# Performance work log

Hardware: AMD Instinct MI355X
Metric: run time of the kernel (lower is better)

Reference implementation:

```python
import jax, jax.numpy as jnp
import numpy as np

N_NODES = 20000
T_STEPS = 8


def _layer_norm(x, g, b, eps=1e-5):
    mu = x.mean(-1, keepdims=True)
    var = ((x - mu) ** 2).mean(-1, keepdims=True)
    return (x - mu) * jax.lax.rsqrt(var + eps) * g + b


def _linear(x, W, b):
    # torch nn.Linear: x @ W.T + b, W is [out, in]
    return x @ W.T + b


def _gcn_conv(xw, norm, src, dst, b, n):
    # xw: pre-transformed features [N, H]; symmetric-normalized aggregation
    msg = xw[src] * norm[:, None]
    return jax.ops.segment_sum(msg, dst, num_segments=n) + b


def setup_inputs() -> dict:
    key = jax.random.key(0)
    ks = jax.random.split(key, 16)
    N, T, K, E, D, H, M = N_NODES, T_STEPS, 4000, 400000, 128, 128, 16
    s = 0.05
    return {
        "node_t": jax.random.randint(ks[0], (T, K), 0, N),
        "edge_index_t": jax.random.randint(ks[1], (T, 2, E), 0, N),
        "m": M,
        "emb": jax.random.normal(ks[2], (N, D), jnp.float32) * s,
        "convW1": jax.random.normal(ks[3], (H, D), jnp.float32) * s,
        "convb1": jnp.zeros((H,), jnp.float32),
        "convW2": jax.random.normal(ks[4], (H, H), jnp.float32) * s,
        "convb2": jnp.zeros((H,), jnp.float32),
        "tn_g": jnp.ones((H,), jnp.float32),
        "tn_b": jnp.zeros((H,), jnp.float32),
        "tok_w1": jax.random.normal(ks[5], (M, M), jnp.float32) * s,
        "tok_b1": jnp.zeros((M,), jnp.float32),
        "tok_w2": jax.random.normal(ks[6], (M, M), jnp.float32) * s,
        "tok_b2": jnp.zeros((M,), jnp.float32),
        "cn_g": jnp.ones((H,), jnp.float32),
        "cn_b": jnp.zeros((H,), jnp.float32),
        "ch_w1": jax.random.normal(ks[7], (H, H), jnp.float32) * s,
        "ch_b1": jnp.zeros((H,), jnp.float32),
        "ch_w2": jax.random.normal(ks[8], (H, H), jnp.float32) * s,
        "ch_b2": jnp.zeros((H,), jnp.float32),
    }


def reference(node_t, edge_index_t, m, emb, convW1, convb1, convW2, convb2,
              tn_g, tn_b, tok_w1, tok_b1, tok_w2, tok_b2,
              cn_g, cn_b, ch_w1, ch_b1, ch_w2, ch_b2):
    N = emb.shape[0]
    H = convW1.shape[0]
    gelu = lambda x: jax.nn.gelu(x, approximate=False)

    def mixer(x):  # x: [N, m, H]
        y = _layer_norm(x, tn_g, tn_b)
        y = jnp.swapaxes(y, 1, 2)                 # [N, H, m]
        y = _linear(gelu(_linear(y, tok_w1, tok_b1)), tok_w2, tok_b2)
        x = x + jnp.swapaxes(y, 1, 2)
        z = _layer_norm(x, cn_g, cn_b)
        z = _linear(gelu(_linear(z, ch_w1, ch_b1)), ch_w2, ch_b2)
        return x + z

    # conv linear transforms are per-node dense and constant w.r.t. step input emb
    xw1 = emb @ convW1.T                          # [N, H]
    self_loop = jnp.arange(N)

    def step(x_m, xs):
        node_i, edge_i = xs                        # [K], [2, E]
        x_m_new = mixer(x_m)
        x_new = x_m_new.mean(axis=1)               # FinalProcessLayer, discrete
        # GCN with self-loops and symmetric normalization
        src = jnp.concatenate([edge_i[0], self_loop])
        dst = jnp.concatenate([edge_i[1], self_loop])
        deg = jax.ops.segment_sum(jnp.ones_like(src, jnp.float32), dst,
                                  num_segments=N)
        dinv = jax.lax.rsqrt(jnp.maximum(deg, 1.0))
        norm = dinv[src] * dinv[dst]
        h = _gcn_conv(xw1, norm, src, dst, convb1, N)
        h = jax.nn.relu(h)
        h = _gcn_conv(h @ convW2.T, norm, src, dst, convb2, N)
        # zero rows of nodes present at this timestep (boolean-mask scatter)
        h = h.at[node_i].set(0.0)
        # slide window
        x_m = jnp.concatenate([x_m[:, 1:, :], h[:, None, :]], axis=1)
        return x_m, x_new

    x_m0 = jnp.zeros((N, m, H), jnp.float32)
    _, outs = jax.lax.scan(step, x_m0, (node_t, edge_index_t))
    return outs  # [T, N, H]
```

## Files before the change

### kernel.cpp

```cpp
#include <hip/hip_runtime.h>
#include <hip/hip_bf16.h>
#include <cstdint>
#include <cstddef>

#define NN 20000
#define HH 128
#define MM 16
#define KK 4000
#define EE 400000

typedef __attribute__((ext_vector_type(16))) float f16v;
typedef __attribute__((ext_vector_type(8))) short short8;
typedef __attribute__((ext_vector_type(4))) float f32x4;
typedef __attribute__((ext_vector_type(8), may_alias)) short s8ma;
typedef __attribute__((ext_vector_type(4), may_alias)) float f4ma;

__device__ __forceinline__ float gelu_f(float x) {
  return 0.5f * x * (1.0f + erff(x * 0.70710678118654752440f));
}

__device__ __forceinline__ unsigned short f2bf(float f) {
  union { float f; unsigned u; } v; v.f = f;
  unsigned u = v.u;
  unsigned r = (u + 0x7FFFu + ((u >> 16) & 1u)) >> 16;
  return (unsigned short)r;
}
__device__ __forceinline__ float bf2f(unsigned short s) {
  union { unsigned u; float f; } v; v.u = ((unsigned)s) << 16; return v.f;
}


__global__ void zero1_kernel(int* __restrict__ a, int n) {
  int i = blockIdx.x * 256 + threadIdx.x;
  if (i < n) a[i] = 0;
}

__global__ void count7_kernel(const int* __restrict__ edges, int* __restrict__ cnt7, int n7) {
  int e = blockIdx.x * 256 + threadIdx.x;
  if (e < n7) {
    int t = e / EE, i = e - t * EE;
    int d = edges[(size_t)t * 2 * EE + EE + i];
    atomicAdd(&cnt7[t * NN + d], 1);
  }
}

__global__ void dinv_kernel(const int* __restrict__ cnt, float* __restrict__ dinv, int n) {
  int i = blockIdx.x * 256 + threadIdx.x;
  if (i < n) dinv[i] = rsqrtf((float)(cnt[i] + 1));
}

__global__ void scan7_kernel(const int* __restrict__ cnt7, int* __restrict__ offs7) {
  __shared__ int sh[1024];
  __shared__ int carry_s;
  const int b = blockIdx.x;
  const int* cnt = cnt7 + b * NN;
  int* offs = offs7 + b * (NN + 1);
  int tid = threadIdx.x;
  if (tid == 0) carry_s = 0;
  __syncthreads();
  for (int base = 0; base < NN; base += 1024) {
    int i = base + tid;
    int v = (i < NN) ? cnt[i] : 0;
    sh[tid] = v;
    __syncthreads();
    for (int off = 1; off < 1024; off <<= 1) {
      int t = (tid >= off) ? sh[tid - off] : 0;
      __syncthreads();
      sh[tid] += t;
      __syncthreads();
    }
    int carry = carry_s;
    if (i < NN) offs[i] = carry + sh[tid] - v;
    __syncthreads();
    if (tid == 1023) carry_s = carry + sh[1023];
    __syncthreads();
  }
  if (tid == 0) offs[NN] = carry_s;
}

__global__ void fillcsr7_kernel(const int* __restrict__ edges,
                                const int* __restrict__ offs7, int* __restrict__ cursor7,
                                const float* __restrict__ dinv7,
                                int* __restrict__ csrc7, float* __restrict__ cnorm7, int n7) {
  int e = blockIdx.x * 256 + threadIdx.x;
  if (e < n7) {
    int t = e / EE, i = e - t * EE;
    const int* es = edges + (size_t)t * 2 * EE;
    int s = es[i], d = es[EE + i];
    int pos = offs7[t * (NN + 1) + d] + atomicAdd(&cursor7[t * NN + d], 1);
    csrc7[(size_t)t * EE + pos] = s;
    cnorm7[(size_t)t * EE + pos] = dinv7[t * NN + s] * dinv7[t * NN + d];
  }
}

__global__ __launch_bounds__(128) void agg7_kernel(const float* __restrict__ X,
    const int* __restrict__ csrc7, const float* __restrict__ cnorm7,
    const int* __restrict__ offs7, const float* __restrict__ dinv7,
    const float* __restrict__ bias, int relu, float* __restrict__ Y, int xshared) {
  const int b = blockIdx.x;
  const int t = b / NN, i = b - t * NN;
  const int c = threadIdx.x;
  const int* csrc = csrc7 + (size_t)t * EE;
  const float* cnorm = cnorm7 + (size_t)t * EE;
  const int* offs = offs7 + t * (NN + 1);
  const float* dinv = dinv7 + t * NN;
  const float* Xt = xshared ? X : X + (size_t)t * NN * HH;
  float di = dinv[i];
  float acc = Xt[(size_t)i * HH + c] * di * di;
  int s0 = offs[i], e0 = offs[i + 1];
  for (int j = s0; j < e0; ++j) {
    acc += Xt[(size_t)csrc[j] * HH + c] * cnorm[j];
  }
  acc += bias[c];
  if (relu) acc = fmaxf(acc, 0.f);
  Y[(size_t)b * HH + c] = acc;
}

__global__ __launch_bounds__(128) void gemm128_kernel(const float* __restrict__ X,
    const float* __restrict__ W, float* __restrict__ Y, int nrows) {
  __shared__ float Ws[128 * 129];
  __shared__ float Xs[8 * 128];
  int tid = threadIdx.x;
  for (int idx = tid; idx < 16384; idx += 128) {
    int o = idx >> 7, k = idx & 127;
    Ws[o * 129 + k] = W[idx];
  }
  __syncthreads();
  for (int row0 = blockIdx.x * 8; row0 < nrows; row0 += gridDim.x * 8) {
    int nr = min(8, nrows - row0);
    for (int idx = tid; idx < nr * 128; idx += 128) Xs[idx] = X[(size_t)row0 * 128 + idx];
    __syncthreads();
    float acc[8] = {0, 0, 0, 0, 0, 0, 0, 0};
    for (int k = 0; k < 128; ++k) {
      float w = Ws[tid * 129 + k];
#pragma unroll
      for (int r = 0; r < 8; ++r) acc[r] += w * Xs[r * 128 + k];
    }
    for (int r = 0; r < nr; ++r) Y[(size_t)(row0 + r) * 128 + tid] = acc[r];
    __syncthreads();
  }
}

__global__ void mask7_kernel(const int* __restrict__ node_t, float* __restrict__ hb, int n) {
  int idx = blockIdx.x * 256 + threadIdx.x;
  if (idx < n) {
    int t = idx / (KK * HH), r = idx - t * KK * HH;
    int j = r >> 7, c = r & 127;
    hb[((size_t)t * NN + node_t[t * KK + j]) * HH + c] = 0.f;
  }
}

__global__ void bcast_kernel(float* __restrict__ out, int total) {
  int idx = blockIdx.x * 256 + threadIdx.x + 128;
  if (idx < total) out[idx] = out[idx & 127];
}

__global__ void wprep_kernel(const float* __restrict__ w1, const float* __restrict__ w2,
                             unsigned short* __restrict__ b1, unsigned short* __restrict__ b2) {
  int i = blockIdx.x * 256 + threadIdx.x;
  if (i < 16384) { b1[i] = f2bf(w1[i]); b2[i] = f2bf(w2[i]); }
}


__global__ __launch_bounds__(256, 2) void mixA_kernel(
    const float* __restrict__ hbufs,
    const float* __restrict__ tn_g, const float* __restrict__ tn_b,
    const float* __restrict__ tok_w1, const float* __restrict__ tok_b1,
    const float* __restrict__ tok_w2, const float* __restrict__ tok_b2,
    const float* __restrict__ cn_g, const float* __restrict__ cn_b,
    unsigned short* __restrict__ zh_g, unsigned short* __restrict__ zl_g,
    float* __restrict__ fout_g, int total_items, int item4s, int niter) {
  __shared__ __align__(16) float zw[64 * 132];
  __shared__ float tg[128], tbv[128], cg[128], cbv[128];
  __shared__ float tw1s[256], tw2s[256], tb1s[16], tb2s[16];

  const int tid = threadIdx.x;
  if (tid < 128) {
    tg[tid] = tn_g[tid]; tbv[tid] = tn_b[tid];
    cg[tid] = cn_g[tid]; cbv[tid] = cn_b[tid];
  }
  tw1s[tid] = tok_w1[tid];
  tw2s[tid] = tok_w2[tid];
  if (tid < 16) { tb1s[tid] = tok_b1[tid]; tb2s[tid] = tok_b2[tid]; }
  __syncthreads();

  const int lr = tid >> 2;
  const int lq = tid & 3;
  const int c2 = tid & 127;
  const int n0 = tid >> 7;

  for (int it = 0; it < niter; ++it) {
    const int item4 = it * gridDim.x + blockIdx.x;
    if (item4 >= item4s) break;

    {
      const int n = lr >> 4, tok = lr & 15;
      const int item = item4 * 4 + n;
      const bool act = item < total_items;
      int t = 0, node = 0;
      if (act && item < 7 * NN) { t = item / NN + 1; node = item % NN; }
      int src_t = tok - (MM - t);
      f4ma x[8];
      if (act && src_t >= 0) {
        const float* hp = hbufs + ((size_t)src_t * NN + node) * HH + lq * 32;
#pragma unroll
        for (int j = 0; j < 8; ++j) x[j] = *(const f4ma*)(hp + 4 * j);
      } else {
#pragma unroll
        for (int j = 0; j < 8; ++j) x[j] = (f4ma){0.f, 0.f, 0.f, 0.f};
      }
      float s = 0.f, ss = 0.f;
#pragma unroll
      for (int j = 0; j < 8; ++j) {
        s += x[j].x + x[j].y + x[j].z + x[j].w;
        ss += x[j].x * x[j].x + x[j].y * x[j].y + x[j].z * x[j].z + x[j].w * x[j].w;
      }
      s += __shfl_xor(s, 1); ss += __shfl_xor(ss, 1);
      s += __shfl_xor(s, 2); ss += __shfl_xor(ss, 2);
      float mu = s * (1.f / 128.f);
      float var = fmaxf(ss * (1.f / 128.f) - mu * mu, 0.f);
      float rs = rsqrtf(var + 1e-5f);
#pragma unroll
      for (int j = 0; j < 8; ++j) *(f4ma*)&zw[lr * 132 + lq * 32 + 4 * j] = x[j];
      if (lq == 0) { zw[lr * 132 + 128] = mu; zw[lr * 132 + 129] = rs; }
    }
    __syncthreads();

    {
      const int rb0 = n0 * 16 * 132, rb1 = (n0 + 2) * 16 * 132;
      const float tgc = tg[c2], tbc = tbv[c2];
      f16v a0v, a1v;
#pragma unroll
      for (int hd = 0; hd < 16; ++hd) { float b = tb1s[hd]; a0v[hd] = b; a1v[hd] = b; }
#pragma unroll
      for (int r = 0; r < 16; ++r) {
        float x0 = zw[rb0 + r * 132 + c2];
        float m0 = zw[rb0 + r * 132 + 128], q0 = zw[rb0 + r * 132 + 129];
        float x1 = zw[rb1 + r * 132 + c2];
        float m1 = zw[rb1 + r * 132 + 128], q1 = zw[rb1 + r * 132 + 129];
        float z0 = (x0 - m0) * q0 * tgc + tbc;
        float z1 = (x1 - m1) * q1 * tgc + tbc;
#pragma unroll
        for (int hd = 0; hd < 16; ++hd) {
          float w = tw1s[hd * 16 + r];
          a0v[hd] += w * z0; a1v[hd] += w * z1;
        }
      }
#pragma unroll
      for (int hd = 0; hd < 16; ++hd) { a0v[hd] = gelu_f(a0v[hd]); a1v[hd] = gelu_f(a1v[hd]); }
      float cs0 = 0.f, cs1 = 0.f;
#pragma unroll
      for (int r = 0; r < 16; ++r) {
        float o0 = tb2s[r], o1 = tb2s[r];
#pragma unroll
        for (int hd = 0; hd < 16; ++hd) {
          float w = tw2s[r * 16 + hd];
          o0 += w * a0v[hd]; o1 += w * a1v[hd];
        }
        float nx0 = zw[rb0 + r * 132 + c2] + o0;
        float nx1 = zw[rb1 + r * 132 + c2] + o1;
        cs0 += nx0; cs1 += nx1;
        zw[rb0 + r * 132 + c2] = nx0;
        zw[rb1 + r * 132 + c2] = nx1;
      }
      fout_g[(size_t)(item4 * 4 + n0) * 128 + c2] = cs0;
      fout_g[(size_t)(item4 * 4 + n0 + 2) * 128 + c2] = cs1;
    }
    __syncthreads();

    {
      f4ma x[8];
#pragma unroll
      for (int j = 0; j < 8; ++j) x[j] = *(const f4ma*)&zw[lr * 132 + lq * 32 + 4 * j];
      float s = 0.f, ss = 0.f;
#pragma unroll
      for (int j = 0; j < 8; ++j) {
        s += x[j].x + x[j].y + x[j].z + x[j].w;
        ss += x[j].x * x[j].x + x[j].y * x[j].y + x[j].z * x[j].z + x[j].w * x[j].w;
      }
      s += __shfl_xor(s, 1); ss += __shfl_xor(ss, 1);
      s += __shfl_xor(s, 2); ss += __shfl_xor(ss, 2);
      float mu = s * (1.f / 128.f);
      float var = fmaxf(ss * (1.f / 128.f) - mu * mu, 0.f);
      float rs = rsqrtf(var + 1e-5f);
      const size_t g0 = (size_t)item4 * 64 * 128 + (size_t)lr * 128;
#pragma unroll
      for (int j = 0; j < 4; ++j) {
        int c0 = lq * 32 + 8 * j;
        short8 ph, pl;
#pragma unroll
        for (int e = 0; e < 8; ++e) {
          int c = c0 + e;
          float xe = (e < 4) ? ((const float*)&x[2 * j])[e] : ((const float*)&x[2 * j + 1])[e - 4];
          float zf = (xe - mu) * rs * cg[c] + cbv[c];
          unsigned short hi = f2bf(zf);
          ph[e] = (short)hi;
          pl[e] = (short)f2bf(zf - bf2f(hi));
        }
        *(s8ma*)&zh_g[g0 + c0] = (s8ma)ph;
        *(s8ma*)&zl_g[g0 + c0] = (s8ma)pl;
      }
    }
    __syncthreads();
  }
}


__global__ __launch_bounds__(256, 2) void mixB_kernel(
    const unsigned short* __restrict__ zh_g, const unsigned short* __restrict__ zl_g,
    const float* __restrict__ fout_g,
    const unsigned short* __restrict__ wbf1, const unsigned short* __restrict__ wbf2,
    const float* __restrict__ ch_b1, const float* __restrict__ ch_b2,
    float* __restrict__ out, int total_items, int item4s, int niter) {
  __shared__ __align__(16) unsigned short zh[64 * 136];
  __shared__ __align__(16) unsigned short zl[64 * 136];
  __shared__ float cb1v[128], cb2v[128];

  const int tid = threadIdx.x;
  const int lane = tid & 63;
  const int wv = tid >> 6;
  const int q = lane >> 4;
  const int h = lane & 15;
  if (tid < 128) { cb1v[tid] = ch_b1[tid]; cb2v[tid] = ch_b2[tid]; }
  __syncthreads();

  const int wbase0 = ((2 * wv) * 16 + h) * 128 + q * 8;
  const int wbase1 = ((2 * wv + 1) * 16 + h) * 128 + q * 8;
  const int srow = tid >> 2;
  const int scq = tid & 3;

  for (int it = 0; it < niter; ++it) {
    const int item4 = it * gridDim.x + blockIdx.x;
    if (item4 >= item4s) break;

    {
      const size_t g0 = (size_t)item4 * 64 * 128 + (size_t)srow * 128 + scq * 32;
#pragma unroll
      for (int j = 0; j < 4; ++j) {
        *(s8ma*)&zh[srow * 136 + scq * 32 + 8 * j] = *(const s8ma*)&zh_g[g0 + 8 * j];
        *(s8ma*)&zl[srow * 136 + scq * 32 + 8 * j] = *(const s8ma*)&zl_g[g0 + 8 * j];
      }
    }
    __syncthreads();

    asm volatile("" ::: "memory");
    {
      short8 wf[4][2];
#pragma unroll
      for (int ks = 0; ks < 4; ++ks) {
        wf[ks][0] = (short8)(*(const s8ma*)&wbf1[wbase0 + ks * 32]);
        wf[ks][1] = (short8)(*(const s8ma*)&wbf1[wbase1 + ks * 32]);
      }
      f32x4 acc[4][2];
#pragma unroll
      for (int rt = 0; rt < 4; ++rt) {
#pragma unroll
        for (int j = 0; j < 2; ++j) {
          float b = cb1v[(2 * wv + j) * 16 + h];
          acc[rt][j] = (f32x4){b, b, b, b};
        }
      }
#pragma unroll
      for (int ks = 0; ks < 4; ++ks) {
        const int col = ks * 32 + q * 8;
#pragma unroll
        for (int rt = 0; rt < 4; ++rt) {
          short8 ah = (short8)(*(const s8ma*)&zh[(rt * 16 + h) * 136 + col]);
          short8 al = (short8)(*(const s8ma*)&zl[(rt * 16 + h) * 136 + col]);
#pragma unroll
          for (int j = 0; j < 2; ++j) {
            acc[rt][j] = __builtin_amdgcn_mfma_f32_16x16x32_bf16(ah, wf[ks][j], acc[rt][j], 0, 0, 0);
            acc[rt][j] = __builtin_amdgcn_mfma_f32_16x16x32_bf16(al, wf[ks][j], acc[rt][j], 0, 0, 0);
          }
        }
      }
      __syncthreads();
#pragma unroll
      for (int rt = 0; rt < 4; ++rt) {
#pragma unroll
        for (int j = 0; j < 2; ++j) {
          int col = (2 * wv + j) * 16 + h;
#pragma unroll
          for (int rg = 0; rg < 4; ++rg) {
            int row = rt * 16 + q * 4 + rg;
            float v = gelu_f(acc[rt][j][rg]);
            unsigned short hi = f2bf(v);
            zh[row * 136 + col] = hi;
            zl[row * 136 + col] = f2bf(v - bf2f(hi));
          }
        }
      }
    }
    __syncthreads();

    asm volatile("" ::: "memory");
    {
      short8 wf[4][2];
#pragma unroll
      for (int ks = 0; ks < 4; ++ks) {
        wf[ks][0] = (short8)(*(const s8ma*)&wbf2[wbase0 + ks * 32]);
        wf[ks][1] = (short8)(*(const s8ma*)&wbf2[wbase1 + ks * 32]);
      }
      f32x4 acc[4][2];
#pragma unroll
      for (int rt = 0; rt < 4; ++rt) {
#pragma unroll
        for (int j = 0; j < 2; ++j) {
          float b = cb2v[(2 * wv + j) * 16 + h];
          acc[rt][j] = (f32x4){b, b, b, b};
        }
      }
#pragma unroll
      for (int ks = 0; ks < 4; ++ks) {
        const int col = ks * 32 + q * 8;
#pragma unroll
        for (int rt = 0; rt < 4; ++rt) {
          short8 ah = (short8)(*(const s8ma*)&zh[(rt * 16 + h) * 136 + col]);
          short8 al = (short8)(*(const s8ma*)&zl[(rt * 16 + h) * 136 + col]);
#pragma unroll
          for (int j = 0; j < 2; ++j) {
            acc[rt][j] = __builtin_amdgcn_mfma_f32_16x16x32_bf16(ah, wf[ks][j], acc[rt][j], 0, 0, 0);
            acc[rt][j] = __builtin_amdgcn_mfma_f32_16x16x32_bf16(al, wf[ks][j], acc[rt][j], 0, 0, 0);
          }
        }
      }
#pragma unroll
      for (int rt = 0; rt < 4; ++rt) {
        const int item = item4 * 4 + rt;
        const bool act = item < total_items;
        int t = 0, node = 0;
        if (act && item < 7 * NN) { t = item / NN + 1; node = item % NN; }
#pragma unroll
        for (int j = 0; j < 2; ++j) {
          float v = acc[rt][j][0] + acc[rt][j][1] + acc[rt][j][2] + acc[rt][j][3];
          v += __shfl_xor(v, 16);
          v += __shfl_xor(v, 32);
          if (q == 0 && act) {
            int col = (2 * wv + j) * 16 + h;
            out[((size_t)t * NN + node) * HH + col] =
                (fout_g[(size_t)item * 128 + col] + v) * (1.f / 16.f);
          }
        }
      }
    }
    __syncthreads();
  }
}


__global__ __launch_bounds__(256) void mixer16_kernel(
    const float* __restrict__ hbufs,
    const float* __restrict__ tn_g, const float* __restrict__ tn_b,
    const float* __restrict__ tok_w1, const float* __restrict__ tok_b1,
    const float* __restrict__ tok_w2, const float* __restrict__ tok_b2,
    const float* __restrict__ cn_g, const float* __restrict__ cn_b,
    const float* __restrict__ ch_w1, const float* __restrict__ ch_b1,
    const float* __restrict__ ch_w2, const float* __restrict__ ch_b2,
    float* __restrict__ out, int total_items, int niter) {
  __shared__ __align__(16) float zw[64 * 132];
  __shared__ __align__(16) unsigned short zh[64 * 136];
  __shared__ __align__(16) unsigned short zl[64 * 136];
  __shared__ float fout[4 * 128];
  __shared__ float tg[128], tbv[128], cg[128], cbv[128], cb1v[128], cb2v[128];
  __shared__ float tw1s[256], tw2s[256], tb1s[16], tb2s[16];

  const int tid = threadIdx.x;
  const int lane = tid & 63;
  const int wv = tid >> 6;
  const int q = lane >> 4;
  const int h = lane & 15;

  if (tid < 128) {
    tg[tid] = tn_g[tid]; tbv[tid] = tn_b[tid];
    cg[tid] = cn_g[tid]; cbv[tid] = cn_b[tid];
    cb1v[tid] = ch_b1[tid]; cb2v[tid] = ch_b2[tid];
  }
  tw1s[tid] = tok_w1[tid];
  tw2s[tid] = tok_w2[tid];
  if (tid < 16) { tb1s[tid] = tok_b1[tid]; tb2s[tid] = tok_b2[tid]; }

  short8 wf1[4][2], wf2[4][2];
#pragma unroll
  for (int ks = 0; ks < 4; ++ks) {
#pragma unroll
    for (int j = 0; j < 2; ++j) {
      int o = (2 * wv + j) * 16 + h;
      int k0 = ks * 32 + q * 8;
      const float* s1 = ch_w1 + o * 128 + k0;
      const float* s2 = ch_w2 + o * 128 + k0;
      short8 p1, p2;
#pragma unroll
      for (int e = 0; e < 8; ++e) { p1[e] = (short)f2bf(s1[e]); p2[e] = (short)f2bf(s2[e]); }
      wf1[ks][j] = p1;
      wf2[ks][j] = p2;
    }
  }
  __syncthreads();

  const int lr = tid >> 2;
  const int lq = tid & 3;
  const int c2 = tid & 127;
  const int n0 = tid >> 7;

  for (int it = 0; it < niter; ++it) {
    const int item4 = it * gridDim.x + blockIdx.x;

    {
      const int n = lr >> 4, tok = lr & 15;
      const int item = item4 * 4 + n;
      const bool act = item < total_items;
      int t = 0, node = 0;
      if (act && item < 7 * NN) { t = item / NN + 1; node = item % NN; }
      int src_t = tok - (MM - t);
      f4ma x[8];
      if (act && src_t >= 0) {
        const float* hp = hbufs + ((size_t)src_t * NN + node) * HH + lq * 32;
#pragma unroll
        for (int j = 0; j < 8; ++j) x[j] = *(const f4ma*)(hp + 4 * j);
      } else {
#pragma unroll
        for (int j = 0; j < 8; ++j) x[j] = (f4ma){0.f, 0.f, 0.f, 0.f};
      }
      float s = 0.f, ss = 0.f;
#pragma unroll
      for (int j = 0; j < 8; ++j) {
        s += x[j].x + x[j].y + x[j].z + x[j].w;
        ss += x[j].x * x[j].x + x[j].y * x[j].y + x[j].z * x[j].z + x[j].w * x[j].w;
      }
      s += __shfl_xor(s, 1); ss += __shfl_xor(ss, 1);
      s += __shfl_xor(s, 2); ss += __shfl_xor(ss, 2);
      float mu = s * (1.f / 128.f);
      float var = fmaxf(ss * (1.f / 128.f) - mu * mu, 0.f);
      float rs = rsqrtf(var + 1e-5f);
#pragma unroll
      for (int j = 0; j < 8; ++j) *(f4ma*)&zw[lr * 132 + lq * 32 + 4 * j] = x[j];
      if (lq == 0) { zw[lr * 132 + 128] = mu; zw[lr * 132 + 129] = rs; }
    }
    __syncthreads();

    {
      const int rb0 = n0 * 16 * 132, rb1 = (n0 + 2) * 16 * 132;
      const float tgc = tg[c2], tbc = tbv[c2];
      f16v a0v, a1v;
#pragma unroll
      for (int hd = 0; hd < 16; ++hd) { float b = tb1s[hd]; a0v[hd] = b; a1v[hd] = b; }
#pragma unroll
      for (int r = 0; r < 16; ++r) {
        float x0 = zw[rb0 + r * 132 + c2];
        float m0 = zw[rb0 + r * 132 + 128], q0 = zw[rb0 + r * 132 + 129];
        float x1 = zw[rb1 + r * 132 + c2];
        float m1 = zw[rb1 + r * 132 + 128], q1 = zw[rb1 + r * 132 + 129];
        float z0 = (x0 - m0) * q0 * tgc + tbc;
        float z1 = (x1 - m1) * q1 * tgc + tbc;
#pragma unroll
        for (int hd = 0; hd < 16; ++hd) {
          float w = tw1s[hd * 16 + r];
          a0v[hd] += w * z0; a1v[hd] += w * z1;
        }
      }
#pragma unroll
      for (int hd = 0; hd < 16; ++hd) { a0v[hd] = gelu_f(a0v[hd]); a1v[hd] = gelu_f(a1v[hd]); }
      float cs0 = 0.f, cs1 = 0.f;
#pragma unroll
      for (int r = 0; r < 16; ++r) {
        float o0 = tb2s[r], o1 = tb2s[r];
#pragma unroll
        for (int hd = 0; hd < 16; ++hd) {
          float w = tw2s[r * 16 + hd];
          o0 += w * a0v[hd]; o1 += w * a1v[hd];
        }
        float nx0 = zw[rb0 + r * 132 + c2] + o0;
        float nx1 = zw[rb1 + r * 132 + c2] + o1;
        cs0 += nx0; cs1 += nx1;
        zw[rb0 + r * 132 + c2] = nx0;
        zw[rb1 + r * 132 + c2] = nx1;
      }
      fout[n0 * 128 + c2] = cs0;
      fout[(n0 + 2) * 128 + c2] = cs1;
    }
    __syncthreads();

    {
      f4ma x[8];
#pragma unroll
      for (int j = 0; j < 8; ++j) x[j] = *(const f4ma*)&zw[lr * 132 + lq * 32 + 4 * j];
      float s = 0.f, ss = 0.f;
#pragma unroll
      for (int j = 0; j < 8; ++j) {
        s += x[j].x + x[j].y + x[j].z + x[j].w;
        ss += x[j].x * x[j].x + x[j].y * x[j].y + x[j].z * x[j].z + x[j].w * x[j].w;
      }
      s += __shfl_xor(s, 1); ss += __shfl_xor(ss, 1);
      s += __shfl_xor(s, 2); ss += __shfl_xor(ss, 2);
      float mu = s * (1.f / 128.f);
      float var = fmaxf(ss * (1.f / 128.f) - mu * mu, 0.f);
      float rs = rsqrtf(var + 1e-5f);
#pragma unroll
      for (int j = 0; j < 4; ++j) {
        int c0 = lq * 32 + 8 * j;
        short8 ph, pl;
#pragma unroll
        for (int e = 0; e < 8; ++e) {
          int c = c0 + e;
          float xe = (e < 4) ? ((const float*)&x[2 * j])[e] : ((const float*)&x[2 * j + 1])[e - 4];
          float zf = (xe - mu) * rs * cg[c] + cbv[c];
          unsigned short hi = f2bf(zf);
          ph[e] = (short)hi;
          pl[e] = (short)f2bf(zf - bf2f(hi));
        }
        *(s8ma*)&zh[lr * 136 + c0] = (s8ma)ph;
        *(s8ma*)&zl[lr * 136 + c0] = (s8ma)pl;
      }
    }
    __syncthreads();

    {
      f32x4 acc[4][2];
#pragma unroll
      for (int rt = 0; rt < 4; ++rt) {
#pragma unroll
        for (int j = 0; j < 2; ++j) {
          float b = cb1v[(2 * wv + j) * 16 + h];
          acc[rt][j] = (f32x4){b, b, b, b};
        }
      }
#pragma unroll
      for (int ks = 0; ks < 4; ++ks) {
        const int col = ks * 32 + q * 8;
#pragma unroll
        for (int rt = 0; rt < 4; ++rt) {
          short8 ah = (short8)(*(const s8ma*)&zh[(rt * 16 + h) * 136 + col]);
          short8 al = (short8)(*(const s8ma*)&zl[(rt * 16 + h) * 136 + col]);
#pragma unroll
          for (int j = 0; j < 2; ++j) {
            acc[rt][j] = __builtin_amdgcn_mfma_f32_16x16x32_bf16(ah, wf1[ks][j], acc[rt][j], 0, 0, 0);
            acc[rt][j] = __builtin_amdgcn_mfma_f32_16x16x32_bf16(al, wf1[ks][j], acc[rt][j], 0, 0, 0);
          }
        }
      }
      __syncthreads();
#pragma unroll
      for (int rt = 0; rt < 4; ++rt) {
#pragma unroll
        for (int j = 0; j < 2; ++j) {
          int col = (2 * wv + j) * 16 + h;
#pragma unroll
          for (int rg = 0; rg < 4; ++rg) {
            int row = rt * 16 + q * 4 + rg;
            float v = gelu_f(acc[rt][j][rg]);
            unsigned short hi = f2bf(v);
            zh[row * 136 + col] = hi;
            zl[row * 136 + col] = f2bf(v - bf2f(hi));
          }
        }
      }
    }
    __syncthreads();

    {
      f32x4 acc[4][2];
#pragma unroll
      for (int rt = 0; rt < 4; ++rt) {
#pragma unroll
        for (int j = 0; j < 2; ++j) {
          float b = cb2v[(2 * wv + j) * 16 + h];
          acc[rt][j] = (f32x4){b, b, b, b};
        }
      }
#pragma unroll
      for (int ks = 0; ks < 4; ++ks) {
        const int col = ks * 32 + q * 8;
#pragma unroll
        for (int rt = 0; rt < 4; ++rt) {
          short8 ah = (short8)(*(const s8ma*)&zh[(rt * 16 + h) * 136 + col]);
          short8 al = (short8)(*(const s8ma*)&zl[(rt * 16 + h) * 136 + col]);
#pragma unroll
          for (int j = 0; j < 2; ++j) {
            acc[rt][j] = __builtin_amdgcn_mfma_f32_16x16x32_bf16(ah, wf2[ks][j], acc[rt][j], 0, 0, 0);
            acc[rt][j] = __builtin_amdgcn_mfma_f32_16x16x32_bf16(al, wf2[ks][j], acc[rt][j], 0, 0, 0);
          }
        }
      }
#pragma unroll
      for (int rt = 0; rt < 4; ++rt) {
        const int item = item4 * 4 + rt;
        const bool act = item < total_items;
        int t = 0, node = 0;
        if (act && item < 7 * NN) { t = item / NN + 1; node = item % NN; }
#pragma unroll
        for (int j = 0; j < 2; ++j) {
          float v = acc[rt][j][0] + acc[rt][j][1] + acc[rt][j][2] + acc[rt][j][3];
          v += __shfl_xor(v, 16);
          v += __shfl_xor(v, 32);
          if (q == 0 && act) {
            int col = (2 * wv + j) * 16 + h;
            out[((size_t)t * NN + node) * HH + col] = (fout[rt * 128 + col] + v) * (1.f / 16.f);
          }
        }
      }
    }
    __syncthreads();
  }
}


extern "C" void kernel_launch(void* const* d_in, const int* in_sizes, int n_in,
                              void* d_out, int out_size, void* d_ws, size_t ws_size,
                              hipStream_t stream) {
  const int* node_t   = (const int*)d_in[0];
  const int* edges    = (const int*)d_in[1];
  const float* emb    = (const float*)d_in[3];
  const float* convW1 = (const float*)d_in[4];
  const float* convb1 = (const float*)d_in[5];
  const float* convW2 = (const float*)d_in[6];
  const float* convb2 = (const float*)d_in[7];
  const float* tn_g   = (const float*)d_in[8];
  const float* tn_b   = (const float*)d_in[9];
  const float* tok_w1 = (const float*)d_in[10];
  const float* tok_b1 = (const float*)d_in[11];
  const float* tok_w2 = (const float*)d_in[12];
  const float* tok_b2 = (const float*)d_in[13];
  const float* cn_g   = (const float*)d_in[14];
  const float* cn_b   = (const float*)d_in[15];
  const float* ch_w1  = (const float*)d_in[16];
  const float* ch_b1  = (const float*)d_in[17];
  const float* ch_w2  = (const float*)d_in[18];
  const float* ch_b2  = (const float*)d_in[19];
  float* out = (float*)d_out;

  char* ws = (char*)d_ws;
  size_t off = 0;
  auto alloc = [&](size_t bytes) -> void* {
    void* p = ws + off;
    off += (bytes + 511) & ~(size_t)511;
    return p;
  };
  float* xw1   = (float*)alloc((size_t)NN * HH * 4);
  float* hbufs = (float*)alloc((size_t)7 * NN * HH * 4);
  int*   cnt7  = (int*)alloc((size_t)7 * NN * 4);
  float* dinv7 = (float*)alloc((size_t)7 * NN * 4);
  int*   offs7 = (int*)alloc((size_t)7 * (NN + 1) * 4);
  int*   cursor7 = (int*)alloc((size_t)7 * NN * 4);
  unsigned short* wbf1 = (unsigned short*)alloc((size_t)16384 * 2);
  unsigned short* wbf2 = (unsigned short*)alloc((size_t)16384 * 2);

  const bool batched = ws_size >= (size_t)260 * 1024 * 1024;
  const bool split   = ws_size >= (size_t)1700 * 1024 * 1024;

  const int total_items = 7 * NN + 1;
  const int item4s = (total_items + 3) / 4;

  gemm128_kernel<<<512, 128, 0, stream>>>(emb, convW1, xw1, NN);
  wprep_kernel<<<64, 256, 0, stream>>>(ch_w1, ch_w2, wbf1, wbf2);

  zero1_kernel<<<(7 * NN + 255) / 256, 256, 0, stream>>>(cnt7, 7 * NN);
  count7_kernel<<<(7 * EE + 255) / 256, 256, 0, stream>>>(edges, cnt7, 7 * EE);
  dinv_kernel<<<(7 * NN + 255) / 256, 256, 0, stream>>>(cnt7, dinv7, 7 * NN);
  scan7_kernel<<<7, 1024, 0, stream>>>(cnt7, offs7);

  if (batched) {
    int*   csrc7  = (int*)alloc((size_t)7 * EE * 4);
    float* cnorm7 = (float*)alloc((size_t)7 * EE * 4);
    float* h7     = (float*)alloc((size_t)7 * NN * HH * 4);
    float* g7     = (float*)alloc((size_t)7 * NN * HH * 4);

    zero1_kernel<<<(7 * NN + 255) / 256, 256, 0, stream>>>(cursor7, 7 * NN);
    fillcsr7_kernel<<<(7 * EE + 255) / 256, 256, 0, stream>>>(edges, offs7, cursor7,
                                                              dinv7, csrc7, cnorm7, 7 * EE);
    agg7_kernel<<<7 * NN, 128, 0, stream>>>(xw1, csrc7, cnorm7, offs7, dinv7,
                                            convb1, 1, h7, 1);
    gemm128_kernel<<<2048, 128, 0, stream>>>(h7, convW2, g7, 7 * NN);
    agg7_kernel<<<7 * NN, 128, 0, stream>>>(g7, csrc7, cnorm7, offs7, dinv7,
                                            convb2, 0, hbufs, 0);
    mask7_kernel<<<(7 * KK * HH + 255) / 256, 256, 0, stream>>>(node_t, hbufs, 7 * KK * HH);
  } else {
    int*   csrc  = (int*)alloc((size_t)EE * 4);
    float* cnorm = (float*)alloc((size_t)EE * 4);
    float* h1    = (float*)alloc((size_t)NN * HH * 4);
    float* g1    = (float*)alloc((size_t)NN * HH * 4);
    for (int t = 0; t < 7; ++t) {
      const int* offs = offs7 + (size_t)t * (NN + 1);
      const float* dinv = dinv7 + (size_t)t * NN;
      zero1_kernel<<<(NN + 255) / 256, 256, 0, stream>>>(cursor7, NN);
      fillcsr7_kernel<<<(EE + 255) / 256, 256, 0, stream>>>(edges + (size_t)t * 2 * EE,
                                                            offs, cursor7, dinv, csrc, cnorm, EE);
      agg7_kernel<<<NN, 128, 0, stream>>>(xw1, csrc, cnorm, offs, dinv, convb1, 1, h1, 1);
      gemm128_kernel<<<512, 128, 0, stream>>>(h1, convW2, g1, NN);
      agg7_kernel<<<NN, 128, 0, stream>>>(g1, csrc, cnorm, offs, dinv, convb2, 0,
                                          hbufs + (size_t)t * NN * HH, 0);
      mask7_kernel<<<(KK * HH + 255) / 256, 256, 0, stream>>>(node_t + (size_t)t * KK,
                                                              hbufs + (size_t)t * NN * HH,
                                                              KK * HH);
    }
  }

  if (split) {
    float* fout_g = (float*)alloc((size_t)item4s * 4 * 128 * 4);
    unsigned short* zh_g = (unsigned short*)alloc((size_t)item4s * 64 * 128 * 2);
    unsigned short* zl_g = (unsigned short*)alloc((size_t)item4s * 64 * 128 * 2);
    const int nblocks = 2048;
    const int niter = (item4s + nblocks - 1) / nblocks;
    mixA_kernel<<<nblocks, 256, 0, stream>>>(hbufs, tn_g, tn_b, tok_w1, tok_b1,
                                             tok_w2, tok_b2, cn_g, cn_b,
                                             zh_g, zl_g, fout_g,
                                             total_items, item4s, niter);
    mixB_kernel<<<nblocks, 256, 0, stream>>>(zh_g, zl_g, fout_g, wbf1, wbf2,
                                             ch_b1, ch_b2, out,
                                             total_items, item4s, niter);
  } else {
    const int nblocks = 2048;
    const int niter = (item4s + nblocks - 1) / nblocks;
    mixer16_kernel<<<nblocks, 256, 0, stream>>>(hbufs, tn_g, tn_b, tok_w1, tok_b1,
                                                tok_w2, tok_b2, cn_g, cn_b, ch_w1, ch_b1,
                                                ch_w2, ch_b2, out, total_items, niter);
  }
  bcast_kernel<<<((NN * HH - 128) + 255) / 256, 256, 0, stream>>>(out, NN * HH);
}
```

Baseline: 3.234 ms.

## Chunk split mixer kernels over reused scratch buffers to enable split path

The split mixA/mixB path used to need a large workspace and otherwise fell back to the fused mixer16 kernel. It now runs in chunks of 4096 item groups per launch pair, storing intermediates in the h7, g7 and cnorm7 scratch buffers that are already dead after the GCN stage. Each block handles one item group instead of a persistent loop, and the initial sync in mixB is removed. This lets the MFMA-based split path run whenever the batched path does, and the chunk-sized intermediates may stay cache-resident, at the cost of more kernel launches.

```diff
diff --git a/kernel.cpp b/kernel.cpp
--- a/kernel.cpp
+++ b/kernel.cpp
@@ -169,7 +169,11 @@
     const float* __restrict__ tok_w2, const float* __restrict__ tok_b2,
     const float* __restrict__ cn_g, const float* __restrict__ cn_b,
     unsigned short* __restrict__ zh_g, unsigned short* __restrict__ zl_g,
-    float* __restrict__ fout_g, int total_items, int item4s, int niter) {
+    float* __restrict__ fout_g, int total_items, int base4, int item4s) {
+  const int item4 = base4 + blockIdx.x;
+  if (item4 >= item4s) return;
+  const int li = blockIdx.x;
+
   __shared__ __align__(16) float zw[64 * 132];
   __shared__ float tg[128], tbv[128], cg[128], cbv[128];
   __shared__ float tw1s[256], tw2s[256], tb1s[16], tb2s[16];
@@ -189,119 +193,113 @@
   const int c2 = tid & 127;
   const int n0 = tid >> 7;
 
-  for (int it = 0; it < niter; ++it) {
-    const int item4 = it * gridDim.x + blockIdx.x;
-    if (item4 >= item4s) break;
-
-    {
-      const int n = lr >> 4, tok = lr & 15;
-      const int item = item4 * 4 + n;
-      const bool act = item < total_items;
-      int t = 0, node = 0;
-      if (act && item < 7 * NN) { t = item / NN + 1; node = item % NN; }
-      int src_t = tok - (MM - t);
-      f4ma x[8];
-      if (act && src_t >= 0) {
-        const float* hp = hbufs + ((size_t)src_t * NN + node) * HH + lq * 32;
-#pragma unroll
-        for (int j = 0; j < 8; ++j) x[j] = *(const f4ma*)(hp + 4 * j);
-      } else {
-#pragma unroll
-        for (int j = 0; j < 8; ++j) x[j] = (f4ma){0.f, 0.f, 0.f, 0.f};
-      }
-      float s = 0.f, ss = 0.f;
-#pragma unroll
-      for (int j = 0; j < 8; ++j) {
-        s += x[j].x + x[j].y + x[j].z + x[j].w;
-        ss += x[j].x * x[j].x + x[j].y * x[j].y + x[j].z * x[j].z + x[j].w * x[j].w;
-      }
-      s += __shfl_xor(s, 1); ss += __shfl_xor(ss, 1);
-      s += __shfl_xor(s, 2); ss += __shfl_xor(ss, 2);
-      float mu = s * (1.f / 128.f);
-      float var = fmaxf(ss * (1.f / 128.f) - mu * mu, 0.f);
-      float rs = rsqrtf(var + 1e-5f);
-#pragma unroll
-      for (int j = 0; j < 8; ++j) *(f4ma*)&zw[lr * 132 + lq * 32 + 4 * j] = x[j];
-      if (lq == 0) { zw[lr * 132 + 128] = mu; zw[lr * 132 + 129] = rs; }
-    }
-    __syncthreads();
-
-    {
-      const int rb0 = n0 * 16 * 132, rb1 = (n0 + 2) * 16 * 132;
-      const float tgc = tg[c2], tbc = tbv[c2];
-      f16v a0v, a1v;
-#pragma unroll
-      for (int hd = 0; hd < 16; ++hd) { float b = tb1s[hd]; a0v[hd] = b; a1v[hd] = b; }
-#pragma unroll
-      for (int r = 0; r < 16; ++r) {
-        float x0 = zw[rb0 + r * 132 + c2];
-        float m0 = zw[rb0 + r * 132 + 128], q0 = zw[rb0 + r * 132 + 129];
-        float x1 = zw[rb1 + r * 132 + c2];
-        float m1 = zw[rb1 + r * 132 + 128], q1 = zw[rb1 + r * 132 + 129];
-        float z0 = (x0 - m0) * q0 * tgc + tbc;
-        float z1 = (x1 - m1) * q1 * tgc + tbc;
-#pragma unroll
-        for (int hd = 0; hd < 16; ++hd) {
-          float w = tw1s[hd * 16 + r];
-          a0v[hd] += w * z0; a1v[hd] += w * z1;
-        }
-      }
-#pragma unroll
-      for (int hd = 0; hd < 16; ++hd) { a0v[hd] = gelu_f(a0v[hd]); a1v[hd] = gelu_f(a1v[hd]); }
-      float cs0 = 0.f, cs1 = 0.f;
-#pragma unroll
-      for (int r = 0; r < 16; ++r) {
-        float o0 = tb2s[r], o1 = tb2s[r];
-#pragma unroll
-        for (int hd = 0; hd < 16; ++hd) {
-          float w = tw2s[r * 16 + hd];
-          o0 += w * a0v[hd]; o1 += w * a1v[hd];
-        }
-        float nx0 = zw[rb0 + r * 132 + c2] + o0;
-        float nx1 = zw[rb1 + r * 132 + c2] + o1;
-        cs0 += nx0; cs1 += nx1;
-        zw[rb0 + r * 132 + c2] = nx0;
-        zw[rb1 + r * 132 + c2] = nx1;
-      }
-      fout_g[(size_t)(item4 * 4 + n0) * 128 + c2] = cs0;
-      fout_g[(size_t)(item4 * 4 + n0 + 2) * 128 + c2] = cs1;
-    }
-    __syncthreads();
-
-    {
-      f4ma x[8];
-#pragma unroll
-      for (int j = 0; j < 8; ++j) x[j] = *(const f4ma*)&zw[lr * 132 + lq * 32 + 4 * j];
-      float s = 0.f, ss = 0.f;
-#pragma unroll
-      for (int j = 0; j < 8; ++j) {
-        s += x[j].x + x[j].y + x[j].z + x[j].w;
-        ss += x[j].x * x[j].x + x[j].y * x[j].y + x[j].z * x[j].z + x[j].w * x[j].w;
-      }
-      s += __shfl_xor(s, 1); ss += __shfl_xor(ss, 1);
-      s += __shfl_xor(s, 2); ss += __shfl_xor(ss, 2);
-      float mu = s * (1.f / 128.f);
-      float var = fmaxf(ss * (1.f / 128.f) - mu * mu, 0.f);
-      float rs = rsqrtf(var + 1e-5f);
-      const size_t g0 = (size_t)item4 * 64 * 128 + (size_t)lr * 128;
-#pragma unroll
-      for (int j = 0; j < 4; ++j) {
-        int c0 = lq * 32 + 8 * j;
-        short8 ph, pl;
-#pragma unroll
-        for (int e = 0; e < 8; ++e) {
-          int c = c0 + e;
-          float xe = (e < 4) ? ((const float*)&x[2 * j])[e] : ((const float*)&x[2 * j + 1])[e - 4];
-          float zf = (xe - mu) * rs * cg[c] + cbv[c];
-          unsigned short hi = f2bf(zf);
-          ph[e] = (short)hi;
-          pl[e] = (short)f2bf(zf - bf2f(hi));
-        }
-        *(s8ma*)&zh_g[g0 + c0] = (s8ma)ph;
-        *(s8ma*)&zl_g[g0 + c0] = (s8ma)pl;
-      }
-    }
-    __syncthreads();
+  {
+    const int n = lr >> 4, tok = lr & 15;
+    const int item = item4 * 4 + n;
+    const bool act = item < total_items;
+    int t = 0, node = 0;
+    if (act && item < 7 * NN) { t = item / NN + 1; node = item % NN; }
+    int src_t = tok - (MM - t);
+    f4ma x[8];
+    if (act && src_t >= 0) {
+      const float* hp = hbufs + ((size_t)src_t * NN + node) * HH + lq * 32;
+#pragma unroll
+      for (int j = 0; j < 8; ++j) x[j] = *(const f4ma*)(hp + 4 * j);
+    } else {
+#pragma unroll
+      for (int j = 0; j < 8; ++j) x[j] = (f4ma){0.f, 0.f, 0.f, 0.f};
+    }
+    float s = 0.f, ss = 0.f;
+#pragma unroll
+    for (int j = 0; j < 8; ++j) {
+      s += x[j].x + x[j].y + x[j].z + x[j].w;
+      ss += x[j].x * x[j].x + x[j].y * x[j].y + x[j].z * x[j].z + x[j].w * x[j].w;
+    }
+    s += __shfl_xor(s, 1); ss += __shfl_xor(ss, 1);
+    s += __shfl_xor(s, 2); ss += __shfl_xor(ss, 2);
+    float mu = s * (1.f / 128.f);
+    float var = fmaxf(ss * (1.f / 128.f) - mu * mu, 0.f);
+    float rs = rsqrtf(var + 1e-5f);
+#pragma unroll
+    for (int j = 0; j < 8; ++j) *(f4ma*)&zw[lr * 132 + lq * 32 + 4 * j] = x[j];
+    if (lq == 0) { zw[lr * 132 + 128] = mu; zw[lr * 132 + 129] = rs; }
+  }
+  __syncthreads();
+
+  {
+    const int rb0 = n0 * 16 * 132, rb1 = (n0 + 2) * 16 * 132;
+    const float tgc = tg[c2], tbc = tbv[c2];
+    f16v a0v, a1v;
+#pragma unroll
+    for (int hd = 0; hd < 16; ++hd) { float b = tb1s[hd]; a0v[hd] = b; a1v[hd] = b; }
+#pragma unroll
+    for (int r = 0; r < 16; ++r) {
+      float x0 = zw[rb0 + r * 132 + c2];
+      float m0 = zw[rb0 + r * 132 + 128], q0 = zw[rb0 + r * 132 + 129];
+      float x1 = zw[rb1 + r * 132 + c2];
+      float m1 = zw[rb1 + r * 132 + 128], q1 = zw[rb1 + r * 132 + 129];
+      float z0 = (x0 - m0) * q0 * tgc + tbc;
+      float z1 = (x1 - m1) * q1 * tgc + tbc;
+#pragma unroll
+      for (int hd = 0; hd < 16; ++hd) {
+        float w = tw1s[hd * 16 + r];
+        a0v[hd] += w * z0; a1v[hd] += w * z1;
+      }
+    }
+#pragma unroll
+    for (int hd = 0; hd < 16; ++hd) { a0v[hd] = gelu_f(a0v[hd]); a1v[hd] = gelu_f(a1v[hd]); }
+    float cs0 = 0.f, cs1 = 0.f;
+#pragma unroll
+    for (int r = 0; r < 16; ++r) {
+      float o0 = tb2s[r], o1 = tb2s[r];
+#pragma unroll
+      for (int hd = 0; hd < 16; ++hd) {
+        float w = tw2s[r * 16 + hd];
+        o0 += w * a0v[hd]; o1 += w * a1v[hd];
+      }
+      float nx0 = zw[rb0 + r * 132 + c2] + o0;
+      float nx1 = zw[rb1 + r * 132 + c2] + o1;
+      cs0 += nx0; cs1 += nx1;
+      zw[rb0 + r * 132 + c2] = nx0;
+      zw[rb1 + r * 132 + c2] = nx1;
+    }
+    fout_g[(size_t)(li * 4 + n0) * 128 + c2] = cs0;
+    fout_g[(size_t)(li * 4 + n0 + 2) * 128 + c2] = cs1;
+  }
+  __syncthreads();
+
+  {
+    f4ma x[8];
+#pragma unroll
+    for (int j = 0; j < 8; ++j) x[j] = *(const f4ma*)&zw[lr * 132 + lq * 32 + 4 * j];
+    float s = 0.f, ss = 0.f;
+#pragma unroll
+    for (int j = 0; j < 8; ++j) {
+      s += x[j].x + x[j].y + x[j].z + x[j].w;
+      ss += x[j].x * x[j].x + x[j].y * x[j].y + x[j].z * x[j].z + x[j].w * x[j].w;
+    }
+    s += __shfl_xor(s, 1); ss += __shfl_xor(ss, 1);
+    s += __shfl_xor(s, 2); ss += __shfl_xor(ss, 2);
+    float mu = s * (1.f / 128.f);
+    float var = fmaxf(ss * (1.f / 128.f) - mu * mu, 0.f);
+    float rs = rsqrtf(var + 1e-5f);
+    const size_t g0 = (size_t)li * 64 * 128 + (size_t)lr * 128;
+#pragma unroll
+    for (int j = 0; j < 4; ++j) {
+      int c0 = lq * 32 + 8 * j;
+      short8 ph, pl;
+#pragma unroll
+      for (int e = 0; e < 8; ++e) {
+        int c = c0 + e;
+        float xe = (e < 4) ? ((const float*)&x[2 * j])[e] : ((const float*)&x[2 * j + 1])[e - 4];
+        float zf = (xe - mu) * rs * cg[c] + cbv[c];
+        unsigned short hi = f2bf(zf);
+        ph[e] = (short)hi;
+        pl[e] = (short)f2bf(zf - bf2f(hi));
+      }
+      *(s8ma*)&zh_g[g0 + c0] = (s8ma)ph;
+      *(s8ma*)&zl_g[g0 + c0] = (s8ma)pl;
+    }
   }
 }
 
@@ -311,7 +309,11 @@
     const float* __restrict__ fout_g,
     const unsigned short* __restrict__ wbf1, const unsigned short* __restrict__ wbf2,
     const float* __restrict__ ch_b1, const float* __restrict__ ch_b2,
-    float* __restrict__ out, int total_items, int item4s, int niter) {
+    float* __restrict__ out, int total_items, int base4, int item4s) {
+  const int item4 = base4 + blockIdx.x;
+  if (item4 >= item4s) return;
+  const int li = blockIdx.x;
+
   __shared__ __align__(16) unsigned short zh[64 * 136];
   __shared__ __align__(16) unsigned short zl[64 * 136];
   __shared__ float cb1v[128], cb2v[128];
@@ -322,128 +324,121 @@
   const int q = lane >> 4;
   const int h = lane & 15;
   if (tid < 128) { cb1v[tid] = ch_b1[tid]; cb2v[tid] = ch_b2[tid]; }
-  __syncthreads();
 
   const int wbase0 = ((2 * wv) * 16 + h) * 128 + q * 8;
   const int wbase1 = ((2 * wv + 1) * 16 + h) * 128 + q * 8;
   const int srow = tid >> 2;
   const int scq = tid & 3;
 
-  for (int it = 0; it < niter; ++it) {
-    const int item4 = it * gridDim.x + blockIdx.x;
-    if (item4 >= item4s) break;
-
-    {
-      const size_t g0 = (size_t)item4 * 64 * 128 + (size_t)srow * 128 + scq * 32;
-#pragma unroll
-      for (int j = 0; j < 4; ++j) {
-        *(s8ma*)&zh[srow * 136 + scq * 32 + 8 * j] = *(const s8ma*)&zh_g[g0 + 8 * j];
-        *(s8ma*)&zl[srow * 136 + scq * 32 + 8 * j] = *(const s8ma*)&zl_g[g0 + 8 * j];
-      }
-    }
-    __syncthreads();
-
-    asm volatile("" ::: "memory");
-    {
-      short8 wf[4][2];
-#pragma unroll
-      for (int ks = 0; ks < 4; ++ks) {
-        wf[ks][0] = (short8)(*(const s8ma*)&wbf1[wbase0 + ks * 32]);
-        wf[ks][1] = (short8)(*(const s8ma*)&wbf1[wbase1 + ks * 32]);
-      }
-      f32x4 acc[4][2];
+  {
+    const size_t g0 = (size_t)li * 64 * 128 + (size_t)srow * 128 + scq * 32;
+#pragma unroll
+    for (int j = 0; j < 4; ++j) {
+      *(s8ma*)&zh[srow * 136 + scq * 32 + 8 * j] = *(const s8ma*)&zh_g[g0 + 8 * j];
+      *(s8ma*)&zl[srow * 136 + scq * 32 + 8 * j] = *(const s8ma*)&zl_g[g0 + 8 * j];
+    }
+  }
+  __syncthreads();
+
+  asm volatile("" ::: "memory");
+  {
+    short8 wf[4][2];
+#pragma unroll
+    for (int ks = 0; ks < 4; ++ks) {
+      wf[ks][0] = (short8)(*(const s8ma*)&wbf1[wbase0 + ks * 32]);
+      wf[ks][1] = (short8)(*(const s8ma*)&wbf1[wbase1 + ks * 32]);
+    }
+    f32x4 acc[4][2];
+#pragma unroll
+    for (int rt = 0; rt < 4; ++rt) {
+#pragma unroll
+      for (int j = 0; j < 2; ++j) {
+        float b = cb1v[(2 * wv + j) * 16 + h];
+        acc[rt][j] = (f32x4){b, b, b, b};
+      }
+    }
+#pragma unroll
+    for (int ks = 0; ks < 4; ++ks) {
+      const int col = ks * 32 + q * 8;
 #pragma unroll
       for (int rt = 0; rt < 4; ++rt) {
+        short8 ah = (short8)(*(const s8ma*)&zh[(rt * 16 + h) * 136 + col]);
+        short8 al = (short8)(*(const s8ma*)&zl[(rt * 16 + h) * 136 + col]);
 #pragma unroll
         for (int j = 0; j < 2; ++j) {
-          float b = cb1v[(2 * wv + j) * 16 + h];
-          acc[rt][j] = (f32x4){b, b, b, b};
-        }
-      }
-#pragma unroll
-      for (int ks = 0; ks < 4; ++ks) {
-        const int col = ks * 32 + q * 8;
-#pragma unroll
-        for (int rt = 0; rt < 4; ++rt) {
-          short8 ah = (short8)(*(const s8ma*)&zh[(rt * 16 + h) * 136 + col]);
-          short8 al = (short8)(*(const s8ma*)&zl[(rt * 16 + h) * 136 + col]);
-#pragma unroll
-          for (int j = 0; j < 2; ++j) {
-            acc[rt][j] = __builtin_amdgcn_mfma_f32_16x16x32_bf16(ah, wf[ks][j], acc[rt][j], 0, 0, 0);
-            acc[rt][j] = __builtin_amdgcn_mfma_f32_16x16x32_bf16(al, wf[ks][j], acc[rt][j], 0, 0, 0);
-          }
-        }
-      }
-      __syncthreads();
+          acc[rt][j] = __builtin_amdgcn_mfma_f32_16x16x32_bf16(ah, wf[ks][j], acc[rt][j], 0, 0, 0);
+          acc[rt][j] = __builtin_amdgcn_mfma_f32_16x16x32_bf16(al, wf[ks][j], acc[rt][j], 0, 0, 0);
+        }
+      }
+    }
+    __syncthreads();
+#pragma unroll
+    for (int rt = 0; rt < 4; ++rt) {
+#pragma unroll
+      for (int j = 0; j < 2; ++j) {
+        int col = (2 * wv + j) * 16 + h;
+#pragma unroll
+        for (int rg = 0; rg < 4; ++rg) {
+          int row = rt * 16 + q * 4 + rg;
+          float v = gelu_f(acc[rt][j][rg]);
+          unsigned short hi = f2bf(v);
+          zh[row * 136 + col] = hi;
+          zl[row * 136 + col] = f2bf(v - bf2f(hi));
+        }
+      }
+    }
+  }
+  __syncthreads();
+
+  asm volatile("" ::: "memory");
+  {
+    short8 wf[4][2];
+#pragma unroll
+    for (int ks = 0; ks < 4; ++ks) {
+      wf[ks][0] = (short8)(*(const s8ma*)&wbf2[wbase0 + ks * 32]);
+      wf[ks][1] = (short8)(*(const s8ma*)&wbf2[wbase1 + ks * 32]);
+    }
+    f32x4 acc[4][2];
+#pragma unroll
+    for (int rt = 0; rt < 4; ++rt) {
+#pragma unroll
+      for (int j = 0; j < 2; ++j) {
+        float b = cb2v[(2 * wv + j) * 16 + h];
+        acc[rt][j] = (f32x4){b, b, b, b};
+      }
+    }
+#pragma unroll
+    for (int ks = 0; ks < 4; ++ks) {
+      const int col = ks * 32 + q * 8;
 #pragma unroll
       for (int rt = 0; rt < 4; ++rt) {
+        short8 ah = (short8)(*(const s8ma*)&zh[(rt * 16 + h) * 136 + col]);
+        short8 al = (short8)(*(const s8ma*)&zl[(rt * 16 + h) * 136 + col]);
 #pragma unroll
         for (int j = 0; j < 2; ++j) {
+          acc[rt][j] = __builtin_amdgcn_mfma_f32_16x16x32_bf16(ah, wf[ks][j], acc[rt][j], 0, 0, 0);
+          acc[rt][j] = __builtin_amdgcn_mfma_f32_16x16x32_bf16(al, wf[ks][j], acc[rt][j], 0, 0, 0);
+        }
+      }
+    }
+#pragma unroll
+    for (int rt = 0; rt < 4; ++rt) {
+      const int item = item4 * 4 + rt;
+      const bool act = item < total_items;
+      int t = 0, node = 0;
+      if (act && item < 7 * NN) { t = item / NN + 1; node = item % NN; }
+#pragma unroll
+      for (int j = 0; j < 2; ++j) {
+        float v = acc[rt][j][0] + acc[rt][j][1] + acc[rt][j][2] + acc[rt][j][3];
+        v += __shfl_xor(v, 16);
+        v += __shfl_xor(v, 32);
+        if (q == 0 && act) {
           int col = (2 * wv + j) * 16 + h;
-#pragma unroll
-          for (int rg = 0; rg < 4; ++rg) {
-            int row = rt * 16 + q * 4 + rg;
-            float v = gelu_f(acc[rt][j][rg]);
-            unsigned short hi = f2bf(v);
-            zh[row * 136 + col] = hi;
-            zl[row * 136 + col] = f2bf(v - bf2f(hi));
-          }
-        }
-      }
-    }
-    __syncthreads();
-
-    asm volatile("" ::: "memory");
-    {
-      short8 wf[4][2];
-#pragma unroll
-      for (int ks = 0; ks < 4; ++ks) {
-        wf[ks][0] = (short8)(*(const s8ma*)&wbf2[wbase0 + ks * 32]);
-        wf[ks][1] = (short8)(*(const s8ma*)&wbf2[wbase1 + ks * 32]);
-      }
-      f32x4 acc[4][2];
-#pragma unroll
-      for (int rt = 0; rt < 4; ++rt) {
-#pragma unroll
-        for (int j = 0; j < 2; ++j) {
-          float b = cb2v[(2 * wv + j) * 16 + h];
-          acc[rt][j] = (f32x4){b, b, b, b};
-        }
-      }
-#pragma unroll
-      for (int ks = 0; ks < 4; ++ks) {
-        const int col = ks * 32 + q * 8;
-#pragma unroll
-        for (int rt = 0; rt < 4; ++rt) {
-          short8 ah = (short8)(*(const s8ma*)&zh[(rt * 16 + h) * 136 + col]);
-          short8 al = (short8)(*(const s8ma*)&zl[(rt * 16 + h) * 136 + col]);
-#pragma unroll
-          for (int j = 0; j < 2; ++j) {
-            acc[rt][j] = __builtin_amdgcn_mfma_f32_16x16x32_bf16(ah, wf[ks][j], acc[rt][j], 0, 0, 0);
-            acc[rt][j] = __builtin_amdgcn_mfma_f32_16x16x32_bf16(al, wf[ks][j], acc[rt][j], 0, 0, 0);
-          }
-        }
-      }
-#pragma unroll
-      for (int rt = 0; rt < 4; ++rt) {
-        const int item = item4 * 4 + rt;
-        const bool act = item < total_items;
-        int t = 0, node = 0;
-        if (act && item < 7 * NN) { t = item / NN + 1; node = item % NN; }
-#pragma unroll
-        for (int j = 0; j < 2; ++j) {
-          float v = acc[rt][j][0] + acc[rt][j][1] + acc[rt][j][2] + acc[rt][j][3];
-          v += __shfl_xor(v, 16);
-          v += __shfl_xor(v, 32);
-          if (q == 0 && act) {
-            int col = (2 * wv + j) * 16 + h;
-            out[((size_t)t * NN + node) * HH + col] =
-                (fout_g[(size_t)item * 128 + col] + v) * (1.f / 16.f);
-          }
-        }
-      }
-    }
-    __syncthreads();
+          out[((size_t)t * NN + node) * HH + col] =
+              (fout_g[(size_t)(li * 4 + rt) * 128 + col] + v) * (1.f / 16.f);
+        }
+      }
+    }
   }
 }
 
@@ -745,7 +740,6 @@
   unsigned short* wbf2 = (unsigned short*)alloc((size_t)16384 * 2);
 
   const bool batched = ws_size >= (size_t)260 * 1024 * 1024;
-  const bool split   = ws_size >= (size_t)1700 * 1024 * 1024;
 
   const int total_items = 7 * NN + 1;
   const int item4s = (total_items + 3) / 4;
@@ -773,6 +767,20 @@
     agg7_kernel<<<7 * NN, 128, 0, stream>>>(g7, csrc7, cnorm7, offs7, dinv7,
                                             convb2, 0, hbufs, 0);
     mask7_kernel<<<(7 * KK * HH + 255) / 256, 256, 0, stream>>>(node_t, hbufs, 7 * KK * HH);
+
+    unsigned short* zh_g = (unsigned short*)h7;
+    unsigned short* zl_g = (unsigned short*)g7;
+    float* fout_g = cnorm7;
+    const int CHUNK = 4096;
+    for (int base4 = 0; base4 < item4s; base4 += CHUNK) {
+      mixA_kernel<<<CHUNK, 256, 0, stream>>>(hbufs, tn_g, tn_b, tok_w1, tok_b1,
+                                             tok_w2, tok_b2, cn_g, cn_b,
+                                             zh_g, zl_g, fout_g,
+                                             total_items, base4, item4s);
+      mixB_kernel<<<CHUNK, 256, 0, stream>>>(zh_g, zl_g, fout_g, wbf1, wbf2,
+                                             ch_b1, ch_b2, out,
+                                             total_items, base4, item4s);
+    }
   } else {
     int*   csrc  = (int*)alloc((size_t)EE * 4);
     float* cnorm = (float*)alloc((size_t)EE * 4);
@@ -792,22 +800,6 @@
                                                               hbufs + (size_t)t * NN * HH,
                                                               KK * HH);
     }
-  }
-
-  if (split) {
-    float* fout_g = (float*)alloc((size_t)item4s * 4 * 128 * 4);
-    unsigned short* zh_g = (unsigned short*)alloc((size_t)item4s * 64 * 128 * 2);
-    unsigned short* zl_g = (unsigned short*)alloc((size_t)item4s * 64 * 128 * 2);
-    const int nblocks = 2048;
-    const int niter = (item4s + nblocks - 1) / nblocks;
-    mixA_kernel<<<nblocks, 256, 0, stream>>>(hbufs, tn_g, tn_b, tok_w1, tok_b1,
-                                             tok_w2, tok_b2, cn_g, cn_b,
-                                             zh_g, zl_g, fout_g,
-                                             total_items, item4s, niter);
-    mixB_kernel<<<nblocks, 256, 0, stream>>>(zh_g, zl_g, fout_g, wbf1, wbf2,
-                                             ch_b1, ch_b2, out,
-                                             total_items, item4s, niter);
-  } else {
     const int nblocks = 2048;
     const int niter = (item4s + nblocks - 1) / nblocks;
     mixer16_kernel<<<nblocks, 256, 0, stream>>>(hbufs, tn_g, tn_b, tok_w1, tok_b1,
```

Result: slower. 3.899 ms (+20.6%).
